# Kernel tuning notes

Measured on AMD Instinct MI355X. Metric: run time of the kernel, lower is better.

The kernel has to match this reference:

```python
import jax, jax.numpy as jnp
import numpy as np

B, N, K = 8, 2048, 64
RADII = (0.1, 0.3, 0.7)
TU = 256   # t_net_units
U = 512    # mmtsc_units
BLK = [(512, 512), (512, 256), (256, 170)]  # pce_depth=3, filters U//(i+1)
EPS = 1e-3  # keras BatchNormalization epsilon
BN_SCALE = np.float32(1.0 / np.sqrt(1.0 + EPS))  # inference BN: mean=0, var=1


def bn(x, g, b):
    return x * (g * BN_SCALE) + b


def setup_inputs():
    key = jax.random.key(0)
    ks = jax.random.split(key, 32)
    r = lambda i, sh, s=0.1: jax.random.normal(ks[i], sh, dtype=jnp.float32) * s
    inp = {
        "points": jax.random.normal(ks[0], (B, N, 3), dtype=jnp.float32),
        "noise": jax.random.uniform(ks[1], (B, N, N), dtype=jnp.float32),
        "tw": r(2, (3, TU)), "tb": r(3, (TU,)),
        "tg1": 1.0 + r(4, (TU,)), "tbt1": r(5, (TU,)),
        "td1w": r(6, (TU, TU)), "td1b": r(7, (TU,)),
        "tg2": 1.0 + r(8, (TU,)), "tbt2": r(9, (TU,)),
        "td2w": r(10, (TU, 9), 0.01), "td2b": jnp.ones((9,), jnp.float32),
        "c1w": r(11, (3 * K * 3, U)), "c1b": r(12, (U,)),
        "g1": 1.0 + r(13, (U,)), "be1": r(14, (U,)),
        "rw": r(15, (U, U)), "rb": r(16, (U,)),
    }
    for i, (ci, co) in enumerate(BLK):
        j = 17 + 4 * i
        inp[f"b{i+1}w"] = r(j, (ci, co))
        inp[f"b{i+1}b"] = r(j + 1, (co,))
        inp[f"b{i+1}g"] = 1.0 + r(j + 2, (co,))
        inp[f"b{i+1}be"] = r(j + 3, (co,))
    return inp


def reference(points, noise, tw, tb, tg1, tbt1, td1w, td1b, tg2, tbt2, td2w, td2b,
              c1w, c1b, g1, be1, rw, rb,
              b1w, b1b, b1g, b1be, b2w, b2b, b2g, b2be, b3w, b3b, b3g, b3be):
    relu = jax.nn.relu
    # ---- T-Net (dropout inactive at inference) ----
    x = relu(bn(points @ tw + tb, tg1, tbt1))       # [B,N,TU] (1x1 conv)
    x = jnp.max(x, axis=1)                          # GlobalMaxPooling1D -> [B,TU]
    x = relu(bn(x @ td1w + td1b, tg2, tbt2))        # [B,TU]
    T = (x @ td2w + td2b).reshape(-1, 3, 3)         # [B,3,3]
    pts = points @ T                                # [B,N,3]
    # ---- pairwise distances + multi-scale ball query ----
    diff = pts[:, :, None, :] - pts[:, None, :, :]  # [B,N,N,3]
    d = jax.lax.stop_gradient(jnp.sqrt(jnp.sum(diff * diff, axis=-1)))  # [B,N,N]
    bidx = jnp.arange(B)[:, None, None]
    groups = []
    for rad in RADII:
        score = jnp.where(d <= rad, noise, 0.0)     # mask * uniform
        idx = jnp.argsort(-score, axis=-1)[:, :, :K]  # descending, top-K  [B,N,K]
        groups.append(pts[bidx, idx])               # gather -> [B,N,K,3]
    feats = jnp.concatenate(groups, axis=-1).reshape(B, N, 3 * K * 3)  # [B,N,576]
    # ---- MLP stack (1x1 convs) ----
    f = relu(bn(feats @ c1w + c1b, g1, be1))        # [B,N,U]
    f = f + (f @ rw + rb)                           # residual
    for w, b_, g, be in ((b1w, b1b, b1g, b1be), (b2w, b2b, b2g, b2be), (b3w, b3b, b3g, b3be)):
        f = relu(bn(f @ w + b_, g, be))
    return jnp.max(f, axis=1)                       # [B,170]
```

## Files before the change

### kernel.cpp

```cpp
#include <hip/hip_runtime.h>
#include <hip/hip_bf16.h>


#define BN_SCALE 0.99950037468777f

typedef short short8 __attribute__((ext_vector_type(8)));
typedef float floatx4 __attribute__((ext_vector_type(4)));

#define OFF_FEATS 0
#define OFF_R1    18874368
#define OFF_W     (OFF_R1 + 16777216)
#define OFF_C1WT  (OFF_W)
#define OFF_RWT   (OFF_C1WT + 589824)
#define OFF_B1WT  (OFF_RWT + 524288)
#define OFF_B2WT  (OFF_B1WT + 524288)
#define OFF_B3WT  (OFF_B2WT + 262144)
#define OFF_PTS   (OFF_B3WT + 131072)
#define OFF_XM    (OFF_PTS + 196608)

__device__ inline short f2bf(float x) {
    __hip_bfloat16 h = __float2bfloat16(x);
    return *reinterpret_cast<short*>(&h);
}
__device__ inline float bf2f(short s) {
    return __uint_as_float(((unsigned)(unsigned short)s) << 16);
}

__device__ inline void convw_seg(const float* src, short* dst, int K, int N, int i) {
    int n = i / K, k = i - n * K;
    float v = (n < N) ? src[(size_t)k * N + n] : 0.f;
    dst[i] = f2bf(v);
}
__global__ __launch_bounds__(256)
void convw5_k(const float* c1w, const float* rw, const float* b1w,
              const float* b2w, const float* b3w,
              short* c1wT, short* rwT, short* b1wT, short* b2wT, short* b3wT) {
    int i = blockIdx.x * 256 + threadIdx.x;
    if (i < 294912)       convw_seg(c1w, c1wT, 576, 512, i);
    else if (i < 557056)  convw_seg(rw,  rwT,  512, 512, i - 294912);
    else if (i < 819200)  convw_seg(b1w, b1wT, 512, 512, i - 557056);
    else if (i < 950272)  convw_seg(b2w, b2wT, 512, 256, i - 819200);
    else                  convw_seg(b3w, b3wT, 256, 170, i - 950272);
}

__global__ __launch_bounds__(256)
void tnet1_k(const float* __restrict__ points, const float* __restrict__ tw,
             const float* __restrict__ tb, const float* __restrict__ tg1,
             const float* __restrict__ tbt1, float* __restrict__ xm) {
    const int b = blockIdx.y;
    const int u = threadIdx.x;
    const float w0 = tw[u], w1 = tw[256 + u], w2 = tw[512 + u];
    const float bi = tb[u];
    const float gs = tg1[u] * BN_SCALE, bt = tbt1[u];
    const float* pb = points + ((size_t)b * 2048 + blockIdx.x * 256) * 3;
    float m = 0.f;
    for (int nn = 0; nn < 256; nn++) {
        float p0 = pb[nn * 3], p1 = pb[nn * 3 + 1], p2 = pb[nn * 3 + 2];
        float v = p0 * w0 + p1 * w1 + p2 * w2 + bi;
        v = fmaxf(v * gs + bt, 0.f);
        m = fmaxf(m, v);
    }
    atomicMax((unsigned int*)(xm + b * 256 + u), __float_as_uint(m));
}

__global__ __launch_bounds__(256)
void tnet2_k(const float* __restrict__ points, const float* __restrict__ xm,
             const float* __restrict__ td1w, const float* __restrict__ td1b,
             const float* __restrict__ tg2, const float* __restrict__ tbt2,
             const float* __restrict__ td2w, const float* __restrict__ td2b,
             float* __restrict__ pts_out) {
    __shared__ float sx[256], sx2[256], sT[9];
    const int b = blockIdx.x;
    const int t = threadIdx.x;
    sx[t] = xm[b * 256 + t];
    __syncthreads();
    float s = td1b[t];
    for (int v = 0; v < 256; v++) s += sx[v] * td1w[v * 256 + t];
    sx2[t] = fmaxf(s * (tg2[t] * BN_SCALE) + tbt2[t], 0.f);
    __syncthreads();
    if (t < 9) {
        float s2 = td2b[t];
        for (int v = 0; v < 256; v++) s2 += sx2[v] * td2w[v * 9 + t];
        sT[t] = s2;
    }
    __syncthreads();
    for (int n = t; n < 2048; n += 256) {
        size_t idx = ((size_t)b * 2048 + n) * 3;
        float p0 = points[idx], p1 = points[idx + 1], p2 = points[idx + 2];
        pts_out[idx]     = p0 * sT[0] + p1 * sT[3] + p2 * sT[6];
        pts_out[idx + 1] = p0 * sT[1] + p1 * sT[4] + p2 * sT[7];
        pts_out[idx + 2] = p0 * sT[2] + p1 * sT[5] + p2 * sT[8];
    }
}


__device__ inline void ins_one(unsigned& llo, unsigned& lhi, unsigned vlo,
                               unsigned vhi, int upaddr, int lane) {
    unsigned long long lv = ((unsigned long long)lhi << 32) | llo;
    unsigned long long vv = ((unsigned long long)vhi << 32) | vlo;
    unsigned long long ltm = __ballot(lv < vv);
    if (ltm) {
        int p = __builtin_ctzll(ltm);
        unsigned uplo = (unsigned)__builtin_amdgcn_ds_bpermute(upaddr, (int)llo);
        unsigned uphi = (unsigned)__builtin_amdgcn_ds_bpermute(upaddr, (int)lhi);
        if (lane >= p) {
            llo = (lane == p) ? vlo : uplo;
            lhi = (lane == p) ? vhi : uphi;
        }
    }
}

__device__ inline void run_q(unsigned& llo, unsigned& lhi, unsigned long long& th,
                             unsigned klo, unsigned khi, unsigned long long qual,
                             int upaddr, int lane) {
    do {
        int src = __builtin_ctzll(qual);
        qual &= qual - 1;
        unsigned vlo = (unsigned)__builtin_amdgcn_readlane((int)klo, src);
        unsigned vhi = (unsigned)__builtin_amdgcn_readlane((int)khi, src);
        ins_one(llo, lhi, vlo, vhi, upaddr, lane);
    } while (qual);
    th = ((unsigned long long)(unsigned)__builtin_amdgcn_readlane((int)lhi, 63) << 32)
         | (unsigned)__builtin_amdgcn_readlane((int)llo, 63);
}

__device__ inline void init_radius(bool in, unsigned nb, unsigned klo, int lane,
                                   int upaddr, unsigned& llo, unsigned& lhi,
                                   unsigned long long& th) {
    unsigned long long inm = __ballot(in);
    int S = 64 - __builtin_popcountll(inm);
    int mbI = __builtin_amdgcn_mbcnt_hi((unsigned)(inm >> 32),
              __builtin_amdgcn_mbcnt_lo((unsigned)inm, 0));
    int mbS = lane - mbI;
    int dst = in ? (S + mbI) : mbS;
    llo = (unsigned)__builtin_amdgcn_ds_permute(dst << 2, in ? 0 : (int)klo);
    lhi = 0;
    if (inm) {
        do {
            int src = __builtin_ctzll(inm);
            inm &= inm - 1;
            unsigned vlo = (unsigned)__builtin_amdgcn_readlane((int)klo, src);
            unsigned vhi = (unsigned)__builtin_amdgcn_readlane((int)nb, src);
            ins_one(llo, lhi, vlo, vhi, upaddr, lane);
        } while (inm);
    }
    th = ((unsigned long long)(unsigned)__builtin_amdgcn_readlane((int)lhi, 63) << 32)
         | (unsigned)__builtin_amdgcn_readlane((int)llo, 63);
}

__global__ __launch_bounds__(1024)
void topk_feats_k(const float* __restrict__ pts, const float* __restrict__ noise,
                  short* __restrict__ feats) {
    __shared__ float sxp[2048], syp[2048], szp[2048];
    const int b = blockIdx.y;
    const int tid = threadIdx.x;
    const int lane = tid & 63;
    const int wave = tid >> 6;
    const int n = blockIdx.x * 16 + wave;
    const float* nrow = noise + ((size_t)b * 2048 + n) * 2048;
    float ncur = nrow[lane];
    float nnxt = nrow[64 + lane];
    for (int i = tid; i < 2048; i += 1024) {
        size_t p = ((size_t)b * 2048 + i) * 3;
        sxp[i] = pts[p];
        syp[i] = pts[p + 1];
        szp[i] = pts[p + 2];
    }
    __syncthreads();
    const float qx = sxp[n], qy = syp[n], qz = szp[n];
    const int upaddr = (lane - 1) << 2;

    unsigned L0lo, L0hi, L1lo, L1hi, L2lo, L2hi;
    unsigned long long th0, th1, th2;

    {
        float dx = qx - sxp[lane], dy = qy - syp[lane], dz = qz - szp[lane];
        float d = sqrtf(dx * dx + dy * dy + dz * dz);
        unsigned nb = __float_as_uint(ncur);
        unsigned klo = 2047 - lane;
        init_radius(d <= 0.1f, nb, klo, lane, upaddr, L0lo, L0hi, th0);
        init_radius(d <= 0.3f, nb, klo, lane, upaddr, L1lo, L1hi, th1);
        init_radius(d <= 0.7f, nb, klo, lane, upaddr, L2lo, L2hi, th2);
    }
    for (int base = 64; base < 2048; base += 64) {
        float cur = nnxt;
        if (base + 64 < 2048) nnxt = nrow[base + 64 + lane];
        const int j = base + lane;
        float dx = qx - sxp[j], dy = qy - syp[j], dz = qz - szp[j];
        float d = sqrtf(dx * dx + dy * dy + dz * dz);
        unsigned nb = __float_as_uint(cur);
        unsigned klo = 2047 - j;
        unsigned k0hi = (d <= 0.1f) ? nb : 0u;
        unsigned k1hi = (d <= 0.3f) ? nb : 0u;
        unsigned k2hi = (d <= 0.7f) ? nb : 0u;
        unsigned long long key0 = ((unsigned long long)k0hi << 32) | klo;
        unsigned long long key1 = ((unsigned long long)k1hi << 32) | klo;
        unsigned long long key2 = ((unsigned long long)k2hi << 32) | klo;
        unsigned long long q0 = __ballot(key0 > th0);
        unsigned long long q1 = __ballot(key1 > th1);
        unsigned long long q2 = __ballot(key2 > th2);
        if (q0) run_q(L0lo, L0hi, th0, klo, k0hi, q0, upaddr, lane);
        if (q1) run_q(L1lo, L1hi, th1, klo, k1hi, q1, upaddr, lane);
        if (q2) run_q(L2lo, L2hi, th2, klo, k2hi, q2, upaddr, lane);
    }

    size_t basef = ((size_t)b * 2048 + n) * 576 + (size_t)lane * 9;
    int j0 = 2047 - (int)(L0lo & 0x7FFu);
    int j1 = 2047 - (int)(L1lo & 0x7FFu);
    int j2 = 2047 - (int)(L2lo & 0x7FFu);
    feats[basef + 0] = f2bf(sxp[j0]);
    feats[basef + 1] = f2bf(syp[j0]);
    feats[basef + 2] = f2bf(szp[j0]);
    feats[basef + 3] = f2bf(sxp[j1]);
    feats[basef + 4] = f2bf(syp[j1]);
    feats[basef + 5] = f2bf(szp[j1]);
    feats[basef + 6] = f2bf(sxp[j2]);
    feats[basef + 7] = f2bf(syp[j2]);
    feats[basef + 8] = f2bf(szp[j2]);
}

template <int EPI>
__global__ __launch_bounds__(256)
void gemm_k(const short* __restrict__ A, const short* __restrict__ BT,
            int K, int Nact,
            const float* __restrict__ bias, const float* __restrict__ gamma,
            const float* __restrict__ beta,
            short* __restrict__ outB, float* __restrict__ outF,
            const short* __restrict__ resid) {
    __shared__ short sA[128 * 40];
    __shared__ short sB[128 * 40];
    const int tid = threadIdx.x;
    const int lane = tid & 63;
    const int wave = tid >> 6;
    const int wm = wave & 1, wn = wave >> 1;
    const int lr = lane & 15, lq = lane >> 4;
    const long m0 = (long)blockIdx.x * 128;
    const long n0 = (long)blockIdx.y * 128;

    floatx4 acc[4][4];
#pragma unroll
    for (int i = 0; i < 4; i++)
#pragma unroll
        for (int j = 0; j < 4; j++) acc[i][j] = (floatx4){0.f, 0.f, 0.f, 0.f};

    for (int k0 = 0; k0 < K; k0 += 32) {
        __syncthreads();
#pragma unroll
        for (int cc = 0; cc < 2; cc++) {
            int c = tid + cc * 256;
            int rr = c >> 2, p = (c & 3) * 8;
            *(uint4*)(&sA[rr * 40 + p]) = *(const uint4*)(A + (m0 + rr) * K + k0 + p);
            *(uint4*)(&sB[rr * 40 + p]) = *(const uint4*)(BT + (n0 + rr) * K + k0 + p);
        }
        __syncthreads();
        short8 af[4], bf[4];
#pragma unroll
        for (int i = 0; i < 4; i++)
            af[i] = *(const short8*)(&sA[(wm * 64 + i * 16 + lr) * 40 + lq * 8]);
#pragma unroll
        for (int j = 0; j < 4; j++)
            bf[j] = *(const short8*)(&sB[(wn * 64 + j * 16 + lr) * 40 + lq * 8]);
#pragma unroll
        for (int i = 0; i < 4; i++)
#pragma unroll
            for (int j = 0; j < 4; j++)
                acc[i][j] = __builtin_amdgcn_mfma_f32_16x16x32_bf16(af[i], bf[j],
                                                                    acc[i][j], 0, 0, 0);
    }

#pragma unroll
    for (int j = 0; j < 4; j++) {
        long col = n0 + wn * 64 + j * 16 + lr;
        if (col >= Nact) continue;
        float bi = bias[col];
        float gs = 0.f, bt = 0.f;
        if (EPI != 1) { gs = gamma[col] * BN_SCALE; bt = beta[col]; }
        float colmax = 0.f;
#pragma unroll
        for (int i = 0; i < 4; i++) {
#pragma unroll
            for (int rg = 0; rg < 4; rg++) {
                long row = m0 + wm * 64 + i * 16 + lq * 4 + rg;
                float v = acc[i][j][rg];
                if (EPI == 1) {
                    v = v + bi + bf2f(resid[row * Nact + col]);
                    outB[row * Nact + col] = f2bf(v);
                } else {
                    v = fmaxf((v + bi) * gs + bt, 0.f);
                    if (EPI == 0) outB[row * Nact + col] = f2bf(v);
                    else colmax = fmaxf(colmax, v);
                }
            }
        }
        if (EPI == 2) {
            colmax = fmaxf(colmax, __shfl_xor(colmax, 16));
            colmax = fmaxf(colmax, __shfl_xor(colmax, 32));
            if (lq == 0) {
                int bb = (int)(m0 >> 11);
                atomicMax((unsigned int*)&outF[bb * 170 + col],
                          __float_as_uint(colmax));
            }
        }
    }
}

extern "C" void kernel_launch(void* const* d_in, const int* in_sizes, int n_in,
                              void* d_out, int out_size, void* d_ws, size_t ws_size,
                              hipStream_t stream) {
    const float* points = (const float*)d_in[0];
    const float* noise  = (const float*)d_in[1];
    const float* tw   = (const float*)d_in[2];
    const float* tb   = (const float*)d_in[3];
    const float* tg1  = (const float*)d_in[4];
    const float* tbt1 = (const float*)d_in[5];
    const float* td1w = (const float*)d_in[6];
    const float* td1b = (const float*)d_in[7];
    const float* tg2  = (const float*)d_in[8];
    const float* tbt2 = (const float*)d_in[9];
    const float* td2w = (const float*)d_in[10];
    const float* td2b = (const float*)d_in[11];
    const float* c1w  = (const float*)d_in[12];
    const float* c1b  = (const float*)d_in[13];
    const float* g1   = (const float*)d_in[14];
    const float* be1  = (const float*)d_in[15];
    const float* rw   = (const float*)d_in[16];
    const float* rb   = (const float*)d_in[17];
    const float* b1w  = (const float*)d_in[18];
    const float* b1b  = (const float*)d_in[19];
    const float* b1g  = (const float*)d_in[20];
    const float* b1be = (const float*)d_in[21];
    const float* b2w  = (const float*)d_in[22];
    const float* b2b  = (const float*)d_in[23];
    const float* b2g  = (const float*)d_in[24];
    const float* b2be = (const float*)d_in[25];
    const float* b3w  = (const float*)d_in[26];
    const float* b3b  = (const float*)d_in[27];
    const float* b3g  = (const float*)d_in[28];
    const float* b3be = (const float*)d_in[29];

    char* ws = (char*)d_ws;
    short* feats = (short*)(ws + OFF_FEATS);
    short* f1    = (short*)(ws + OFF_R1);
    short* f2    = feats;
    short* f3    = (short*)(ws + OFF_R1);
    short* f4    = feats;
    short* c1wT  = (short*)(ws + OFF_C1WT);
    short* rwT   = (short*)(ws + OFF_RWT);
    short* b1wT  = (short*)(ws + OFF_B1WT);
    short* b2wT  = (short*)(ws + OFF_B2WT);
    short* b3wT  = (short*)(ws + OFF_B3WT);
    float* pts   = (float*)(ws + OFF_PTS);
    float* xm    = (float*)(ws + OFF_XM);

    hipMemsetAsync(xm, 0, 8 * 256 * sizeof(float), stream);
    hipMemsetAsync(d_out, 0, (size_t)out_size * sizeof(float), stream);

    convw5_k<<<3968, 256, 0, stream>>>(c1w, rw, b1w, b2w, b3w,
                                       c1wT, rwT, b1wT, b2wT, b3wT);

    tnet1_k<<<dim3(8, 8), 256, 0, stream>>>(points, tw, tb, tg1, tbt1, xm);
    tnet2_k<<<8, 256, 0, stream>>>(points, xm, td1w, td1b, tg2, tbt2, td2w, td2b, pts);
    topk_feats_k<<<dim3(128, 8), 1024, 0, stream>>>(pts, noise, feats);

    gemm_k<0><<<dim3(128, 4), 256, 0, stream>>>(feats, c1wT, 576, 512, c1b, g1, be1,
                                                f1, nullptr, nullptr);
    gemm_k<1><<<dim3(128, 4), 256, 0, stream>>>(f1, rwT, 512, 512, rb, nullptr, nullptr,
                                                f2, nullptr, f1);
    gemm_k<0><<<dim3(128, 4), 256, 0, stream>>>(f2, b1wT, 512, 512, b1b, b1g, b1be,
                                                f3, nullptr, nullptr);
    gemm_k<0><<<dim3(128, 2), 256, 0, stream>>>(f3, b2wT, 512, 256, b2b, b2g, b2be,
                                                f4, nullptr, nullptr);
    gemm_k<2><<<dim3(128, 2), 256, 0, stream>>>(f4, b3wT, 256, 170, b3b, b3g, b3be,
                                                nullptr, (float*)d_out, nullptr);
}
```

Before: 479.8 us.

## Tile weight transpose, drop atomics in T-Net, use direct global-to-LDS GEMM loads

Several changes land together. The weight conversion now uses a 64x64 shared-memory tiled transpose so both reads and writes are coalesced. The first T-Net kernel stages points in LDS and writes per-block partial maxima instead of atomics, which removes a memset; the second T-Net kernel uses 1024 threads to split the dense-layer reductions. The GEMM tile loads switch to global_load_lds with an unpadded 32-short row stride, which skips the register round trip but may add LDS bank conflicts when fragments are read.

```diff
diff --git a/kernel.cpp b/kernel.cpp
--- a/kernel.cpp
+++ b/kernel.cpp
@@ -6,6 +6,9 @@
 
 typedef short short8 __attribute__((ext_vector_type(8)));
 typedef float floatx4 __attribute__((ext_vector_type(4)));
+
+typedef __attribute__((address_space(1))) const short gshort;
+typedef __attribute__((address_space(3))) short lshort;
 
 #define OFF_FEATS 0
 #define OFF_R1    18874368
@@ -16,7 +19,7 @@
 #define OFF_B2WT  (OFF_B1WT + 524288)
 #define OFF_B3WT  (OFF_B2WT + 262144)
 #define OFF_PTS   (OFF_B3WT + 131072)
-#define OFF_XM    (OFF_PTS + 196608)
+#define OFF_PART  (OFF_PTS + 196608)
 
 __device__ inline short f2bf(float x) {
     __hip_bfloat16 h = __float2bfloat16(x);
@@ -26,65 +29,111 @@
     return __uint_as_float(((unsigned)(unsigned short)s) << 16);
 }
 
-__device__ inline void convw_seg(const float* src, short* dst, int K, int N, int i) {
-    int n = i / K, k = i - n * K;
-    float v = (n < N) ? src[(size_t)k * N + n] : 0.f;
-    dst[i] = f2bf(v);
-}
 __global__ __launch_bounds__(256)
-void convw5_k(const float* c1w, const float* rw, const float* b1w,
-              const float* b2w, const float* b3w,
-              short* c1wT, short* rwT, short* b1wT, short* b2wT, short* b3wT) {
-    int i = blockIdx.x * 256 + threadIdx.x;
-    if (i < 294912)       convw_seg(c1w, c1wT, 576, 512, i);
-    else if (i < 557056)  convw_seg(rw,  rwT,  512, 512, i - 294912);
-    else if (i < 819200)  convw_seg(b1w, b1wT, 512, 512, i - 557056);
-    else if (i < 950272)  convw_seg(b2w, b2wT, 512, 256, i - 819200);
-    else                  convw_seg(b3w, b3wT, 256, 170, i - 950272);
+void convw_t_k(const float* __restrict__ c1w, const float* __restrict__ rw,
+               const float* __restrict__ b1w, const float* __restrict__ b2w,
+               const float* __restrict__ b3w,
+               short* __restrict__ c1wT, short* __restrict__ rwT,
+               short* __restrict__ b1wT, short* __restrict__ b2wT,
+               short* __restrict__ b3wT) {
+    __shared__ float tile[64][65];
+    int bid = blockIdx.x;
+    const float* src; short* dst; int K, N, t;
+    if (bid < 72)       { src = c1w; dst = c1wT; K = 576; N = 512; t = bid; }
+    else if (bid < 136) { src = rw;  dst = rwT;  K = 512; N = 512; t = bid - 72; }
+    else if (bid < 200) { src = b1w; dst = b1wT; K = 512; N = 512; t = bid - 136; }
+    else if (bid < 232) { src = b2w; dst = b2wT; K = 512; N = 256; t = bid - 200; }
+    else                { src = b3w; dst = b3wT; K = 256; N = 170; t = bid - 232; }
+    int ktiles = K >> 6;
+    int k0 = (t % ktiles) * 64, n0 = (t / ktiles) * 64;
+    int tx = threadIdx.x & 63, ty = threadIdx.x >> 6;
+#pragma unroll
+    for (int p = 0; p < 16; p++) {
+        int r = p * 4 + ty;
+        int n = n0 + tx;
+        tile[r][tx] = (n < N) ? src[(size_t)(k0 + r) * N + n] : 0.f;
+    }
+    __syncthreads();
+#pragma unroll
+    for (int p = 0; p < 16; p++) {
+        int r = p * 4 + ty;
+        dst[(size_t)(n0 + r) * K + k0 + tx] = f2bf(tile[tx][r]);
+    }
 }
 
 __global__ __launch_bounds__(256)
 void tnet1_k(const float* __restrict__ points, const float* __restrict__ tw,
              const float* __restrict__ tb, const float* __restrict__ tg1,
-             const float* __restrict__ tbt1, float* __restrict__ xm) {
+             const float* __restrict__ tbt1, float* __restrict__ part) {
+    __shared__ float spts[768];
     const int b = blockIdx.y;
     const int u = threadIdx.x;
+    const float* pb = points + ((size_t)b * 2048 + blockIdx.x * 256) * 3;
+    for (int i = u; i < 768; i += 256) spts[i] = pb[i];
     const float w0 = tw[u], w1 = tw[256 + u], w2 = tw[512 + u];
     const float bi = tb[u];
     const float gs = tg1[u] * BN_SCALE, bt = tbt1[u];
-    const float* pb = points + ((size_t)b * 2048 + blockIdx.x * 256) * 3;
+    __syncthreads();
     float m = 0.f;
     for (int nn = 0; nn < 256; nn++) {
-        float p0 = pb[nn * 3], p1 = pb[nn * 3 + 1], p2 = pb[nn * 3 + 2];
-        float v = p0 * w0 + p1 * w1 + p2 * w2 + bi;
+        float v = spts[nn * 3] * w0 + spts[nn * 3 + 1] * w1 +
+                  spts[nn * 3 + 2] * w2 + bi;
         v = fmaxf(v * gs + bt, 0.f);
         m = fmaxf(m, v);
     }
-    atomicMax((unsigned int*)(xm + b * 256 + u), __float_as_uint(m));
-}
-
-__global__ __launch_bounds__(256)
-void tnet2_k(const float* __restrict__ points, const float* __restrict__ xm,
+    part[((b * 8 + blockIdx.x) << 8) + u] = m;
+}
+
+__global__ __launch_bounds__(1024)
+void tnet2_k(const float* __restrict__ points, const float* __restrict__ part,
              const float* __restrict__ td1w, const float* __restrict__ td1b,
              const float* __restrict__ tg2, const float* __restrict__ tbt2,
              const float* __restrict__ td2w, const float* __restrict__ td2b,
              float* __restrict__ pts_out) {
-    __shared__ float sx[256], sx2[256], sT[9];
+    __shared__ float sx[256], sp[4][256], sx2[256], sp2[9][32], sT[9];
     const int b = blockIdx.x;
-    const int t = threadIdx.x;
-    sx[t] = xm[b * 256 + t];
-    __syncthreads();
-    float s = td1b[t];
-    for (int v = 0; v < 256; v++) s += sx[v] * td1w[v * 256 + t];
-    sx2[t] = fmaxf(s * (tg2[t] * BN_SCALE) + tbt2[t], 0.f);
-    __syncthreads();
-    if (t < 9) {
-        float s2 = td2b[t];
-        for (int v = 0; v < 256; v++) s2 += sx2[v] * td2w[v * 9 + t];
-        sT[t] = s2;
-    }
-    __syncthreads();
-    for (int n = t; n < 2048; n += 256) {
+    const int tid = threadIdx.x;
+    if (tid < 256) {
+        float m = 0.f;
+#pragma unroll
+        for (int c = 0; c < 8; c++) m = fmaxf(m, part[((b * 8 + c) << 8) + tid]);
+        sx[tid] = m;
+    }
+    __syncthreads();
+    {
+        int t = tid & 255, g = tid >> 8;
+        float s = 0.f;
+#pragma unroll 8
+        for (int i = 0; i < 64; i++) {
+            int v = g * 64 + i;
+            s += sx[v] * td1w[v * 256 + t];
+        }
+        sp[g][t] = s;
+    }
+    __syncthreads();
+    if (tid < 256) {
+        float s = td1b[tid] + sp[0][tid] + sp[1][tid] + sp[2][tid] + sp[3][tid];
+        sx2[tid] = fmaxf(s * (tg2[tid] * BN_SCALE) + tbt2[tid], 0.f);
+    }
+    __syncthreads();
+    if (tid < 288) {
+        int j = tid / 32, vg = tid & 31;
+        float s = 0.f;
+#pragma unroll
+        for (int i = 0; i < 8; i++) {
+            int v = vg * 8 + i;
+            s += sx2[v] * td2w[v * 9 + j];
+        }
+        sp2[j][vg] = s;
+    }
+    __syncthreads();
+    if (tid < 9) {
+        float s = td2b[tid];
+        for (int vg = 0; vg < 32; vg++) s += sp2[tid][vg];
+        sT[tid] = s;
+    }
+    __syncthreads();
+    for (int n = tid; n < 2048; n += 1024) {
         size_t idx = ((size_t)b * 2048 + n) * 3;
         float p0 = points[idx], p1 = points[idx + 1], p2 = points[idx + 2];
         pts_out[idx]     = p0 * sT[0] + p1 * sT[3] + p2 * sT[6];
@@ -92,7 +141,6 @@
         pts_out[idx + 2] = p0 * sT[2] + p1 * sT[5] + p2 * sT[8];
     }
 }
-
 
 __device__ inline void ins_one(unsigned& llo, unsigned& lhi, unsigned vlo,
                                unsigned vhi, int upaddr, int lane) {
@@ -172,7 +220,6 @@
 
     unsigned L0lo, L0hi, L1lo, L1hi, L2lo, L2hi;
     unsigned long long th0, th1, th2;
-
     {
         float dx = qx - sxp[lane], dy = qy - syp[lane], dz = qz - szp[lane];
         float d = sqrtf(dx * dx + dy * dy + dz * dz);
@@ -203,7 +250,6 @@
         if (q1) run_q(L1lo, L1hi, th1, klo, k1hi, q1, upaddr, lane);
         if (q2) run_q(L2lo, L2hi, th2, klo, k2hi, q2, upaddr, lane);
     }
-
     size_t basef = ((size_t)b * 2048 + n) * 576 + (size_t)lane * 9;
     int j0 = 2047 - (int)(L0lo & 0x7FFu);
     int j1 = 2047 - (int)(L1lo & 0x7FFu);
@@ -227,8 +273,8 @@
             const float* __restrict__ beta,
             short* __restrict__ outB, float* __restrict__ outF,
             const short* __restrict__ resid) {
-    __shared__ short sA[128 * 40];
-    __shared__ short sB[128 * 40];
+    __shared__ short sA[128 * 32];
+    __shared__ short sB[128 * 32];
     const int tid = threadIdx.x;
     const int lane = tid & 63;
     const int wave = tid >> 6;
@@ -237,6 +283,9 @@
     const long m0 = (long)blockIdx.x * 128;
     const long n0 = (long)blockIdx.y * 128;
 
+    const int srow = (lane >> 2);
+    const int sp8 = (lane & 3) * 8;
+
     floatx4 acc[4][4];
 #pragma unroll
     for (int i = 0; i < 4; i++)
@@ -246,20 +295,24 @@
     for (int k0 = 0; k0 < K; k0 += 32) {
         __syncthreads();
 #pragma unroll
-        for (int cc = 0; cc < 2; cc++) {
-            int c = tid + cc * 256;
-            int rr = c >> 2, p = (c & 3) * 8;
-            *(uint4*)(&sA[rr * 40 + p]) = *(const uint4*)(A + (m0 + rr) * K + k0 + p);
-            *(uint4*)(&sB[rr * 40 + p]) = *(const uint4*)(BT + (n0 + rr) * K + k0 + p);
+        for (int c = 0; c < 2; c++) {
+            int chunk = wave * 2 + c;
+            int rr = chunk * 16 + srow;
+            __builtin_amdgcn_global_load_lds(
+                (gshort*)(A + (m0 + rr) * K + k0 + sp8),
+                (lshort*)&sA[chunk * 512], 16, 0, 0);
+            __builtin_amdgcn_global_load_lds(
+                (gshort*)(BT + (n0 + rr) * K + k0 + sp8),
+                (lshort*)&sB[chunk * 512], 16, 0, 0);
         }
         __syncthreads();
         short8 af[4], bf[4];
 #pragma unroll
         for (int i = 0; i < 4; i++)
-            af[i] = *(const short8*)(&sA[(wm * 64 + i * 16 + lr) * 40 + lq * 8]);
+            af[i] = *(const short8*)(&sA[(wm * 64 + i * 16 + lr) * 32 + lq * 8]);
 #pragma unroll
         for (int j = 0; j < 4; j++)
-            bf[j] = *(const short8*)(&sB[(wn * 64 + j * 16 + lr) * 40 + lq * 8]);
+            bf[j] = *(const short8*)(&sB[(wn * 64 + j * 16 + lr) * 32 + lq * 8]);
 #pragma unroll
         for (int i = 0; i < 4; i++)
 #pragma unroll
@@ -350,16 +403,15 @@
     short* b2wT  = (short*)(ws + OFF_B2WT);
     short* b3wT  = (short*)(ws + OFF_B3WT);
     float* pts   = (float*)(ws + OFF_PTS);
-    float* xm    = (float*)(ws + OFF_XM);
-
-    hipMemsetAsync(xm, 0, 8 * 256 * sizeof(float), stream);
+    float* part  = (float*)(ws + OFF_PART);
+
     hipMemsetAsync(d_out, 0, (size_t)out_size * sizeof(float), stream);
 
-    convw5_k<<<3968, 256, 0, stream>>>(c1w, rw, b1w, b2w, b3w,
+    convw_t_k<<<248, 256, 0, stream>>>(c1w, rw, b1w, b2w, b3w,
                                        c1wT, rwT, b1wT, b2wT, b3wT);
-
-    tnet1_k<<<dim3(8, 8), 256, 0, stream>>>(points, tw, tb, tg1, tbt1, xm);
-    tnet2_k<<<8, 256, 0, stream>>>(points, xm, td1w, td1b, tg2, tbt2, td2w, td2b, pts);
+    tnet1_k<<<dim3(8, 8), 256, 0, stream>>>(points, tw, tb, tg1, tbt1, part);
+    tnet2_k<<<8, 1024, 0, stream>>>(points, part, td1w, td1b, tg2, tbt2,
+                                    td2w, td2b, pts);
     topk_feats_k<<<dim3(128, 8), 1024, 0, stream>>>(pts, noise, feats);
 
     gemm_k<0><<<dim3(128, 4), 256, 0, stream>>>(feats, c1wT, 576, 512, c1b, g1, be1,
```

Measured after the change: 445.1 us. 7.2% less time.
